# Kernel tuning notes

Hardware: AMD Instinct MI355X
Metric: run time of the kernel (lower is better)

## Reference

```python
import jax, jax.numpy as jnp
import numpy as np

N = 20000      # nodes (atoms)
E = 200000     # directed edges
T = 800000     # triplets
H = 128        # hidden_channels
INT = 64       # int_emb_size
BAS = 8        # basis_emb_size
NS = 7         # num_spherical
NR = 6         # num_radial
OUT = 256      # out_emb_channels
NB = 4         # num_blocks
L = 3          # num_output_layers
CUT = 5.0      # cutoff
silu = jax.nn.silu  # 'swish' activation

# Envelope with exponent=5 -> p=6
_P = 6.0
_A = -(_P + 1.0) * (_P + 2.0) / 2.0   # -28
_B = _P * (_P + 2.0)                  # 48
_C = -_P * (_P + 1.0) / 2.0           # -21

def _envelope(d):
    d5 = d ** 5
    return (1.0 / d + _A * d5 + _B * d5 * d + _C * d5 * d * d) * (d < 1.0).astype(d.dtype)

def setup_inputs() -> dict:
    key = jax.random.key(0)
    ks = iter(jax.random.split(key, 64))
    def p(shape, scale=0.05):
        return jax.random.normal(next(ks), shape, dtype=jnp.float32) * scale
    inp = {}
    inp['z'] = jax.random.randint(next(ks), (N,), 0, 95)
    inp['dist'] = jax.random.uniform(next(ks), (E,), minval=0.1, maxval=CUT, dtype=jnp.float32)
    inp['sbf'] = p((T, NS * NR), 1.0)
    inp['i'] = jax.random.randint(next(ks), (E,), 0, N)
    inp['j'] = jax.random.randint(next(ks), (E,), 0, N)
    inp['idx_kj'] = jax.random.randint(next(ks), (T,), 0, E)
    inp['idx_ji'] = jax.random.randint(next(ks), (T,), 0, E)
    # embedding block params
    s3 = float(np.sqrt(3.0))
    inp['emb_table'] = jax.random.uniform(next(ks), (95, H), minval=-s3, maxval=s3, dtype=jnp.float32)
    inp['W_rbf_emb'] = p((NR, H)); inp['b_rbf_emb'] = jnp.zeros((H,), jnp.float32)
    inp['W_emb'] = p((3 * H, H)); inp['b_emb'] = jnp.zeros((H,), jnp.float32)
    inp['freq'] = jnp.arange(1, NR + 1, dtype=jnp.float32) * jnp.pi
    # interaction blocks (stacked over NB)
    inp['Wi_rbf1'] = p((NB, NR, BAS)); inp['Wi_rbf2'] = p((NB, BAS, H))
    inp['Wi_sbf1'] = p((NB, NS * NR, BAS)); inp['Wi_sbf2'] = p((NB, BAS, INT))
    inp['Wi_kj'] = p((NB, H, H)); inp['bi_kj'] = jnp.zeros((NB, H), jnp.float32)
    inp['Wi_ji'] = p((NB, H, H)); inp['bi_ji'] = jnp.zeros((NB, H), jnp.float32)
    inp['Wi_down'] = p((NB, H, INT)); inp['Wi_up'] = p((NB, INT, H))
    inp['Wi_rb_W1'] = p((NB, H, H)); inp['Wi_rb_b1'] = jnp.zeros((NB, H), jnp.float32)
    inp['Wi_rb_W2'] = p((NB, H, H)); inp['Wi_rb_b2'] = jnp.zeros((NB, H), jnp.float32)
    inp['Wi_lin'] = p((NB, H, H)); inp['bi_lin'] = jnp.zeros((NB, H), jnp.float32)
    inp['Wi_ra_W1'] = p((NB, H, H)); inp['Wi_ra_b1'] = jnp.zeros((NB, H), jnp.float32)
    inp['Wi_ra_W2'] = p((NB, H, H)); inp['Wi_ra_b2'] = jnp.zeros((NB, H), jnp.float32)
    # output blocks (stacked over NB+1)
    inp['Wo_rbf'] = p((NB + 1, NR, H)); inp['Wo_up'] = p((NB + 1, H, OUT))
    inp['Wo_linW'] = p((NB + 1, L, OUT, OUT)); inp['Wo_linb'] = jnp.zeros((NB + 1, L, OUT), jnp.float32)
    return inp

def _forward(z, dist, sbf, i, j, idx_kj, idx_ji,
             emb_table, W_rbf_emb, b_rbf_emb, W_emb, b_emb, freq,
             Wi_rbf1, Wi_rbf2, Wi_sbf1, Wi_sbf2, Wi_kj, bi_kj, Wi_ji, bi_ji,
             Wi_down, Wi_up, Wi_rb_W1, Wi_rb_b1, Wi_rb_W2, Wi_rb_b2,
             Wi_lin, bi_lin, Wi_ra_W1, Wi_ra_b1, Wi_ra_W2, Wi_ra_b2,
             Wo_rbf, Wo_up, Wo_linW, Wo_linb):
    num_nodes = z.shape[0]
    num_edges = dist.shape[0]
    # BesselBasisLayer: rbf [E, NR]
    d = dist / CUT
    rbf = _envelope(d)[:, None] * jnp.sin(freq * d[:, None])
    # EmbeddingBlock -> edge features x [E, H]
    h = emb_table[z]
    rbf_h = silu(rbf @ W_rbf_emb + b_rbf_emb)
    x = silu(jnp.concatenate([h[i], h[j], rbf_h], axis=-1) @ W_emb + b_emb)

    def out_block(b, x_e):
        t = (rbf @ Wo_rbf[b]) * x_e                      # [E, H]
        node = jax.ops.segment_sum(t, i, num_segments=num_nodes)
        node = node @ Wo_up[b]                            # [N, OUT]
        for l in range(L):
            node = silu(node @ Wo_linW[b, l] + Wo_linb[b, l])
        return node

    P = out_block(0, x)
    for b in range(NB):
        # InteractionPPBlock
        x_ji = silu(x @ Wi_ji[b] + bi_ji[b])
        x_kj = silu(x @ Wi_kj[b] + bi_kj[b])
        rbf_b = (rbf @ Wi_rbf1[b]) @ Wi_rbf2[b]           # [E, H]
        x_kj = x_kj * rbf_b
        x_kj = silu(x_kj @ Wi_down[b])                    # [E, INT]
        sbf_b = (sbf @ Wi_sbf1[b]) @ Wi_sbf2[b]           # [T, INT]
        x_kj = x_kj[idx_kj] * sbf_b                       # gather triplets
        x_kj = jax.ops.segment_sum(x_kj, idx_ji, num_segments=num_edges)
        x_kj = silu(x_kj @ Wi_up[b])                      # [E, H]
        hdd = x_ji + x_kj
        # one residual layer before skip (num_before_skip=1)
        hdd = hdd + silu(silu(hdd @ Wi_rb_W1[b] + Wi_rb_b1[b]) @ Wi_rb_W2[b] + Wi_rb_b2[b])
        hdd = silu(hdd @ Wi_lin[b] + bi_lin[b]) + x
        # one residual layer after skip (source uses num_before_skip here too)
        hdd = hdd + silu(silu(hdd @ Wi_ra_W1[b] + Wi_ra_b1[b]) @ Wi_ra_W2[b] + Wi_ra_b2[b])
        x = hdd
        P = P + out_block(b + 1, x)
    return P  # [N, OUT] per-node output embeddings

def reference(z, dist, sbf, i, j, idx_kj, idx_ji,
              emb_table, W_rbf_emb, b_rbf_emb, W_emb, b_emb, freq,
              Wi_rbf1, Wi_rbf2, Wi_sbf1, Wi_sbf2, Wi_kj, bi_kj, Wi_ji, bi_ji,
              Wi_down, Wi_up, Wi_rb_W1, Wi_rb_b1, Wi_rb_W2, Wi_rb_b2,
              Wi_lin, bi_lin, Wi_ra_W1, Wi_ra_b1, Wi_ra_W2, Wi_ra_b2,
              Wo_rbf, Wo_up, Wo_linW, Wo_linb):
    return _forward(z, dist, sbf, i, j, idx_kj, idx_ji,
                    emb_table, W_rbf_emb, b_rbf_emb, W_emb, b_emb, freq,
                    Wi_rbf1, Wi_rbf2, Wi_sbf1, Wi_sbf2, Wi_kj, bi_kj, Wi_ji, bi_ji,
                    Wi_down, Wi_up, Wi_rb_W1, Wi_rb_b1, Wi_rb_W2, Wi_rb_b2,
                    Wi_lin, bi_lin, Wi_ra_W1, Wi_ra_b1, Wi_ra_W2, Wi_ra_b2,
                    Wo_rbf, Wo_up, Wo_linW, Wo_linb)
```

## Files before the change

### kernel.cpp

```cpp
#include <hip/hip_runtime.h>
#include <hip/hip_bf16.h>

#define NND 20000
#define NE  200000
#define NT  800000

#define SW256(row) (((row) & 7) << 4)
#define SW128(row) (((row) & 7) << 4)

typedef short  s16x8 __attribute__((ext_vector_type(8)));
typedef float  f32x4 __attribute__((ext_vector_type(4)));

__device__ __forceinline__ float silu_f(float v) {
    return v * __builtin_amdgcn_rcpf(1.0f + __expf(-v));
}

__device__ __forceinline__ ushort f2bf(float f) {
    uint u = __float_as_uint(f);
    uint r = (u + 0x7FFFu + ((u >> 16) & 1u)) >> 16;
    return (ushort)r;
}
__device__ __forceinline__ float bf2f(ushort u) {
    return __uint_as_float(((uint)u) << 16);
}
__device__ __forceinline__ uint f2bf_pk(float a, float b) {
    __hip_bfloat162 h = __float22bfloat162_rn(make_float2(a, b));
    return *(uint*)&h;
}
__device__ __forceinline__ void store_bf4(void* p, float v0, float v1, float v2, float v3) {
    uint2 o;
    o.x = f2bf_pk(v0, v1);
    o.y = f2bf_pk(v2, v3);
    *(uint2*)p = o;
}

__global__ void rbf_kernel(const float* __restrict__ dist, const float* __restrict__ freq,
                           float* __restrict__ rbf, int E)
{
    int e = blockIdx.x * blockDim.x + threadIdx.x;
    if (e >= E) return;
    float d = dist[e] * 0.2f;
    float d5 = d * d; d5 = d5 * d5 * d;
    float env = 1.0f / d + (-28.0f) * d5 + 48.0f * d5 * d + (-21.0f) * d5 * d * d;
    env = (d < 1.0f) ? env : 0.0f;
    float fr[6];
    #pragma unroll
    for (int r = 0; r < 6; ++r) fr[r] = freq[r];
    #pragma unroll
    for (int r = 0; r < 6; ++r)
        rbf[(size_t)e * 6 + r] = env * sinf(fr[r] * d);
}

__global__ void twt_kernel(const float* __restrict__ W, ushort* __restrict__ Wt,
                           int CIN, int COUT, int total)
{
    int idx = blockIdx.x * 256 + threadIdx.x;
    if (idx >= total) return;
    int per = CIN * COUT;
    int b = idx / per, r = idx % per;
    int k = r / COUT, c = r % COUT;
    Wt[(size_t)b * per + (size_t)c * CIN + k] = f2bf(W[idx]);
}

__global__ void twt7_kernel(const float* __restrict__ s0, const float* __restrict__ s1,
                            const float* __restrict__ s2, const float* __restrict__ s3,
                            const float* __restrict__ s4, const float* __restrict__ s5,
                            const float* __restrict__ s6, ushort* __restrict__ dst)
{
    int idx = blockIdx.x * 256 + threadIdx.x;
    int which = idx >> 16;
    int r = idx & 65535;
    const float* s = (which == 0) ? s0 : (which == 1) ? s1 : (which == 2) ? s2 :
                     (which == 3) ? s3 : (which == 4) ? s4 : (which == 5) ? s5 : s6;
    int b = r >> 14;
    int rr = r & 16383;
    int k = rr >> 7, c = rr & 127;
    dst[(size_t)which * 65536 + b * 16384 + c * 128 + k] = f2bf(s[r]);
}

template<int CIN, int COUT, int MODE, typename IT, typename ET, typename OT>
__global__ __launch_bounds__(256) void mfma_lin_kernel(
    const IT* __restrict__ x, const ushort* __restrict__ Wt,
    const float* __restrict__ bias, const ET* __restrict__ extra,
    OT* __restrict__ y, int M)
{
    constexpr int MT = 64;
    constexpr int NF = COUT / 16;
    constexpr int KS = CIN / 32;
    constexpr int PITCH = CIN * 2;
    __shared__ ushort As_u[MT * CIN];
    __shared__ ushort Ws_u[COUT * CIN];
    char* As = (char*)As_u;
    char* Ws = (char*)Ws_u;
    const int tid = threadIdx.x;
    const int row0 = blockIdx.x * MT;
    const bool full = (row0 + MT <= M);

    constexpr int ACH = MT * CIN / 8;
    for (int c = tid; c < ACH; c += 256) {
        int row = c / (CIN / 8);
        int kc  = c % (CIN / 8);
        int grow = row0 + row;
        s16x8 v;
        if (full || grow < M) {
            if constexpr (sizeof(IT) == 4) {
                const float* src = (const float*)x + (size_t)grow * CIN + kc * 8;
                float4 f0 = *(const float4*)(src);
                float4 f1 = *(const float4*)(src + 4);
                v[0] = (short)f2bf(f0.x); v[1] = (short)f2bf(f0.y);
                v[2] = (short)f2bf(f0.z); v[3] = (short)f2bf(f0.w);
                v[4] = (short)f2bf(f1.x); v[5] = (short)f2bf(f1.y);
                v[6] = (short)f2bf(f1.z); v[7] = (short)f2bf(f1.w);
            } else {
                v = *(const s16x8*)((const ushort*)x + (size_t)grow * CIN + kc * 8);
            }
        } else {
            #pragma unroll
            for (int u = 0; u < 8; ++u) v[u] = 0;
        }
        *(s16x8*)(As + ((row * PITCH + kc * 16) ^ SW256(row))) = v;
    }
    constexpr int WCH = COUT * CIN / 8;
    for (int c = tid; c < WCH; c += 256) {
        int col = c / (CIN / 8);
        int kc  = c % (CIN / 8);
        s16x8 v = *(const s16x8*)(Wt + (size_t)col * CIN + kc * 8);
        *(s16x8*)(Ws + ((col * PITCH + kc * 16) ^ SW256(col))) = v;
    }
    __syncthreads();

    const int w = tid >> 6, lane = tid & 63;
    const int l15 = lane & 15, l4 = lane >> 4;
    const int arow = w * 16 + l15;

    f32x4 acc[NF];
    #pragma unroll
    for (int nf = 0; nf < NF; ++nf) acc[nf] = (f32x4){0.f, 0.f, 0.f, 0.f};

    #pragma unroll
    for (int ks = 0; ks < KS; ++ks) {
        const int kbyte = (ks * 32 + l4 * 8) * 2;
        s16x8 a = *(const s16x8*)(As + ((arow * PITCH + kbyte) ^ SW256(arow)));
        #pragma unroll
        for (int nf = 0; nf < NF; ++nf) {
            int col = nf * 16 + l15;
            s16x8 bf = *(const s16x8*)(Ws + ((col * PITCH + kbyte) ^ SW256(col)));
            acc[nf] = __builtin_amdgcn_mfma_f32_16x16x32_bf16(bf, a, acc[nf], 0, 0, 0);
        }
    }

    const int grow = row0 + w * 16 + l15;
    if (grow < M) {
        #pragma unroll
        for (int nf = 0; nf < NF; ++nf) {
            int c0 = nf * 16 + l4 * 4;
            float4 bv = make_float4(0.f, 0.f, 0.f, 0.f);
            if (bias) bv = *(const float4*)(bias + c0);
            float v0 = acc[nf][0] + bv.x, v1 = acc[nf][1] + bv.y;
            float v2 = acc[nf][2] + bv.z, v3 = acc[nf][3] + bv.w;
            if constexpr (MODE & 1) {
                v0 = silu_f(v0); v1 = silu_f(v1); v2 = silu_f(v2); v3 = silu_f(v3);
            }
            if constexpr ((MODE & 4) != 0) {
                if constexpr (sizeof(ET) == 4) {
                    float4 ex = *(const float4*)((const float*)extra + (size_t)grow * COUT + c0);
                    v0 += ex.x; v1 += ex.y; v2 += ex.z; v3 += ex.w;
                } else {
                    ushort4 ex = *(const ushort4*)((const ushort*)extra + (size_t)grow * COUT + c0);
                    v0 += bf2f(ex.x); v1 += bf2f(ex.y); v2 += bf2f(ex.z); v3 += bf2f(ex.w);
                }
            }
            if constexpr (sizeof(OT) == 4) {
                float* o = (float*)y + (size_t)grow * COUT + c0;
                if constexpr (MODE & 8) {
                    float4 cur = *(const float4*)o;
                    v0 += cur.x; v1 += cur.y; v2 += cur.z; v3 += cur.w;
                }
                *(float4*)o = make_float4(v0, v1, v2, v3);
            } else {
                store_bf4((ushort*)y + (size_t)grow * COUT + c0, v0, v1, v2, v3);
            }
        }
    }
}

__global__ __launch_bounds__(256) void mfma_front_kernel(
    const ushort* __restrict__ x,
    const ushort* __restrict__ Wt1, const ushort* __restrict__ Wt2,
    const ushort* __restrict__ Wtd,
    const float* __restrict__ b1, const float* __restrict__ b2,
    const float* __restrict__ rbf, const float* __restrict__ W1r,
    const float* __restrict__ W2r,
    ushort* __restrict__ y1, ushort* __restrict__ yd, int M)
{
    constexpr int PITCH = 256;
    __shared__ ushort A_u[64 * 128];
    __shared__ ushort W1_u[128 * 128];
    __shared__ ushort W2_u[128 * 128];
    char* A = (char*)A_u;
    char* W1s = (char*)W1_u;
    char* W2s = (char*)W2_u;
    const int tid = threadIdx.x;
    const int row0 = blockIdx.x * 64;

    for (int c = tid; c < 1024; c += 256) {
        int row = c >> 4, kc = c & 15;
        s16x8 v = *(const s16x8*)(x + (size_t)(row0 + row) * 128 + kc * 8);
        *(s16x8*)(A + ((row * PITCH + kc * 16) ^ SW256(row))) = v;
    }
    for (int c = tid; c < 2048; c += 256) {
        int col = c >> 4, kc = c & 15;
        int o = (col * PITCH + kc * 16) ^ SW256(col);
        *(s16x8*)(W1s + o) = *(const s16x8*)(Wt1 + (size_t)col * 128 + kc * 8);
        *(s16x8*)(W2s + o) = *(const s16x8*)(Wt2 + (size_t)col * 128 + kc * 8);
    }
    s16x8 wdreg[4];
    #pragma unroll
    for (int i = 0; i < 4; ++i) {
        int c = tid + i * 256;
        wdreg[i] = *(const s16x8*)(Wtd + (size_t)(c >> 4) * 128 + (c & 15) * 8);
    }
    __syncthreads();

    const int w = tid >> 6, lane = tid & 63;
    const int l15 = lane & 15, l4 = lane >> 4;
    const int arow = w * 16 + l15;

    f32x4 acc1[8], acc2[8];
    #pragma unroll
    for (int nf = 0; nf < 8; ++nf) {
        acc1[nf] = (f32x4){0.f, 0.f, 0.f, 0.f};
        acc2[nf] = (f32x4){0.f, 0.f, 0.f, 0.f};
    }
    #pragma unroll
    for (int ks = 0; ks < 4; ++ks) {
        const int kbyte = (ks * 32 + l4 * 8) * 2;
        s16x8 a = *(const s16x8*)(A + ((arow * PITCH + kbyte) ^ SW256(arow)));
        #pragma unroll
        for (int nf = 0; nf < 8; ++nf) {
            int col = nf * 16 + l15;
            int o = (col * PITCH + kbyte) ^ SW256(col);
            s16x8 bf1 = *(const s16x8*)(W1s + o);
            s16x8 bf2 = *(const s16x8*)(W2s + o);
            acc1[nf] = __builtin_amdgcn_mfma_f32_16x16x32_bf16(bf1, a, acc1[nf], 0, 0, 0);
            acc2[nf] = __builtin_amdgcn_mfma_f32_16x16x32_bf16(bf2, a, acc2[nf], 0, 0, 0);
        }
    }
    __syncthreads();

    const int grow = row0 + arow;
    float rv[6];
    #pragma unroll
    for (int q = 0; q < 6; ++q) rv[q] = rbf[(size_t)grow * 6 + q];
    float t8[8];
    #pragma unroll
    for (int p = 0; p < 8; ++p) {
        float s = 0.f;
        #pragma unroll
        for (int q = 0; q < 6; ++q) s += rv[q] * W1r[q * 8 + p];
        t8[p] = s;
    }
    #pragma unroll
    for (int nf = 0; nf < 8; ++nf) {
        int c0 = nf * 16 + l4 * 4;
        float4 bb1 = *(const float4*)(b1 + c0);
        float4 bb2 = *(const float4*)(b2 + c0);
        store_bf4(y1 + (size_t)grow * 128 + c0,
                  silu_f(acc1[nf][0] + bb1.x), silu_f(acc1[nf][1] + bb1.y),
                  silu_f(acc1[nf][2] + bb1.z), silu_f(acc1[nf][3] + bb1.w));
        float r0 = 0.f, r1 = 0.f, r2 = 0.f, r3 = 0.f;
        #pragma unroll
        for (int p = 0; p < 8; ++p) {
            float4 wq = *(const float4*)(W2r + p * 128 + c0);
            float tp = t8[p];
            r0 += tp * wq.x; r1 += tp * wq.y; r2 += tp * wq.z; r3 += tp * wq.w;
        }
        store_bf4(A + ((arow * PITCH + c0 * 2) ^ SW256(arow)),
                  silu_f(acc2[nf][0] + bb2.x) * r0, silu_f(acc2[nf][1] + bb2.y) * r1,
                  silu_f(acc2[nf][2] + bb2.z) * r2, silu_f(acc2[nf][3] + bb2.w) * r3);
    }
    #pragma unroll
    for (int i = 0; i < 4; ++i) {
        int c = tid + i * 256;
        int col = c >> 4, kc = c & 15;
        *(s16x8*)(W1s + ((col * PITCH + kc * 16) ^ SW256(col))) = wdreg[i];
    }
    __syncthreads();

    f32x4 accd[4];
    #pragma unroll
    for (int nf = 0; nf < 4; ++nf) accd[nf] = (f32x4){0.f, 0.f, 0.f, 0.f};
    #pragma unroll
    for (int ks = 0; ks < 4; ++ks) {
        const int kbyte = (ks * 32 + l4 * 8) * 2;
        s16x8 a = *(const s16x8*)(A + ((arow * PITCH + kbyte) ^ SW256(arow)));
        #pragma unroll
        for (int nf = 0; nf < 4; ++nf) {
            int col = nf * 16 + l15;
            s16x8 bf = *(const s16x8*)(W1s + ((col * PITCH + kbyte) ^ SW256(col)));
            accd[nf] = __builtin_amdgcn_mfma_f32_16x16x32_bf16(bf, a, accd[nf], 0, 0, 0);
        }
    }
    #pragma unroll
    for (int nf = 0; nf < 4; ++nf) {
        int c0 = nf * 16 + l4 * 4;
        store_bf4(yd + (size_t)grow * 64 + c0,
                  silu_f(accd[nf][0]), silu_f(accd[nf][1]),
                  silu_f(accd[nf][2]), silu_f(accd[nf][3]));
    }
}

__global__ __launch_bounds__(256) void mfma_back_kernel(
    const ushort* __restrict__ go, const ushort* __restrict__ xji,
    const ushort* __restrict__ x,
    const ushort* __restrict__ Wup, const ushort* __restrict__ Wrb1,
    const ushort* __restrict__ Wrb2, const ushort* __restrict__ Wlin,
    const ushort* __restrict__ Wra1, const ushort* __restrict__ Wra2,
    const float* __restrict__ b_rb1, const float* __restrict__ b_rb2,
    const float* __restrict__ b_lin, const float* __restrict__ b_ra1,
    const float* __restrict__ b_ra2,
    ushort* __restrict__ xout, int M)
{
    __shared__ ushort A_u[64 * 128];
    __shared__ ushort T_u[64 * 128];
    char* A  = (char*)A_u;
    char* Tb = (char*)T_u;
    const int tid = threadIdx.x;
    const int row0 = blockIdx.x * 64;
    const int w = tid >> 6, lane = tid & 63;
    const int l15 = lane & 15, l4 = lane >> 4;
    const int colbase = w * 32;

    f32x4 acc[8];
    s16x8 wfA[8], wfB[8];
    ushort4 xr[8];

    auto zero_acc = [&]() {
        #pragma unroll
        for (int i = 0; i < 8; ++i) acc[i] = (f32x4){0.f, 0.f, 0.f, 0.f};
    };
    auto load_w8 = [&](s16x8* wf, const ushort* Wg) {
        #pragma unroll
        for (int nfi = 0; nfi < 2; ++nfi)
            #pragma unroll
            for (int ks = 0; ks < 4; ++ks)
                wf[nfi * 4 + ks] = *(const s16x8*)(
                    Wg + (size_t)(colbase + nfi * 16 + l15) * 128 + ks * 32 + l4 * 8);
    };
    auto load_rows = [&](const ushort* src) {
        #pragma unroll
        for (int rt = 0; rt < 4; ++rt) {
            int grow = row0 + rt * 16 + l15;
            #pragma unroll
            for (int nfi = 0; nfi < 2; ++nfi) {
                int c0 = colbase + nfi * 16 + l4 * 4;
                xr[rt * 2 + nfi] = *(const ushort4*)(src + (size_t)grow * 128 + c0);
            }
        }
    };
    auto run_phase = [&](char* Ab, const s16x8* wf) {
        #pragma unroll
        for (int rt = 0; rt < 4; ++rt) {
            int row = rt * 16 + l15;
            #pragma unroll
            for (int ks = 0; ks < 4; ++ks) {
                s16x8 a = *(const s16x8*)(Ab + ((row * 256 + ks * 64 + l4 * 16) ^ SW256(row)));
                acc[rt * 2 + 0] = __builtin_amdgcn_mfma_f32_16x16x32_bf16(wf[0 * 4 + ks], a, acc[rt * 2 + 0], 0, 0, 0);
                acc[rt * 2 + 1] = __builtin_amdgcn_mfma_f32_16x16x32_bf16(wf[1 * 4 + ks], a, acc[rt * 2 + 1], 0, 0, 0);
            }
        }
    };

    s16x8 wfUp[4];
    #pragma unroll
    for (int nfi = 0; nfi < 2; ++nfi)
        #pragma unroll
        for (int ks = 0; ks < 2; ++ks)
            wfUp[nfi * 2 + ks] = *(const s16x8*)(
                Wup + (size_t)(colbase + nfi * 16 + l15) * 64 + ks * 32 + l4 * 8);
    for (int c = tid; c < 512; c += 256) {
        int row = c >> 3, kc = c & 7;
        s16x8 v = *(const s16x8*)(go + (size_t)(row0 + row) * 64 + kc * 8);
        *(s16x8*)(Tb + ((row * 128 + kc * 16) ^ SW128(row))) = v;
    }
    load_w8(wfA, Wrb1);
    load_rows(xji);
    __syncthreads();

    zero_acc();
    #pragma unroll
    for (int rt = 0; rt < 4; ++rt) {
        int row = rt * 16 + l15;
        #pragma unroll
        for (int ks = 0; ks < 2; ++ks) {
            s16x8 a = *(const s16x8*)(Tb + ((row * 128 + ks * 64 + l4 * 16) ^ SW128(row)));
            acc[rt * 2 + 0] = __builtin_amdgcn_mfma_f32_16x16x32_bf16(wfUp[0 * 2 + ks], a, acc[rt * 2 + 0], 0, 0, 0);
            acc[rt * 2 + 1] = __builtin_amdgcn_mfma_f32_16x16x32_bf16(wfUp[1 * 2 + ks], a, acc[rt * 2 + 1], 0, 0, 0);
        }
    }
    #pragma unroll
    for (int rt = 0; rt < 4; ++rt) {
        int row = rt * 16 + l15;
        #pragma unroll
        for (int nfi = 0; nfi < 2; ++nfi) {
            int c0 = colbase + nfi * 16 + l4 * 4;
            f32x4 v = acc[rt * 2 + nfi];
            ushort4 xj = xr[rt * 2 + nfi];
            store_bf4(A + ((row * 256 + c0 * 2) ^ SW256(row)),
                      bf2f(xj.x) + silu_f(v[0]), bf2f(xj.y) + silu_f(v[1]),
                      bf2f(xj.z) + silu_f(v[2]), bf2f(xj.w) + silu_f(v[3]));
        }
    }
    __syncthreads();

    load_w8(wfB, Wrb2);
    zero_acc();
    run_phase(A, wfA);
    #pragma unroll
    for (int rt = 0; rt < 4; ++rt) {
        int row = rt * 16 + l15;
        #pragma unroll
        for (int nfi = 0; nfi < 2; ++nfi) {
            int c0 = colbase + nfi * 16 + l4 * 4;
            f32x4 v = acc[rt * 2 + nfi];
            float4 bb = *(const float4*)(b_rb1 + c0);
            store_bf4(Tb + ((row * 256 + c0 * 2) ^ SW256(row)),
                      silu_f(v[0] + bb.x), silu_f(v[1] + bb.y),
                      silu_f(v[2] + bb.z), silu_f(v[3] + bb.w));
        }
    }
    __syncthreads();

    load_w8(wfA, Wlin);
    load_rows(x);
    zero_acc();
    run_phase(Tb, wfB);
    #pragma unroll
    for (int rt = 0; rt < 4; ++rt) {
        int row = rt * 16 + l15;
        #pragma unroll
        for (int nfi = 0; nfi < 2; ++nfi) {
            int c0 = colbase + nfi * 16 + l4 * 4;
            f32x4 v = acc[rt * 2 + nfi];
            float4 bb = *(const float4*)(b_rb2 + c0);
            int ao = (row * 256 + c0 * 2) ^ SW256(row);
            ushort4 h = *(const ushort4*)(A + ao);
            store_bf4(A + ao,
                      bf2f(h.x) + silu_f(v[0] + bb.x), bf2f(h.y) + silu_f(v[1] + bb.y),
                      bf2f(h.z) + silu_f(v[2] + bb.z), bf2f(h.w) + silu_f(v[3] + bb.w));
        }
    }
    __syncthreads();

    load_w8(wfB, Wra1);
    zero_acc();
    run_phase(A, wfA);
    __syncthreads();
    #pragma unroll
    for (int rt = 0; rt < 4; ++rt) {
        int row = rt * 16 + l15;
        #pragma unroll
        for (int nfi = 0; nfi < 2; ++nfi) {
            int c0 = colbase + nfi * 16 + l4 * 4;
            f32x4 v = acc[rt * 2 + nfi];
            float4 bb = *(const float4*)(b_lin + c0);
            ushort4 xv = xr[rt * 2 + nfi];
            store_bf4(A + ((row * 256 + c0 * 2) ^ SW256(row)),
                      silu_f(v[0] + bb.x) + bf2f(xv.x), silu_f(v[1] + bb.y) + bf2f(xv.y),
                      silu_f(v[2] + bb.z) + bf2f(xv.z), silu_f(v[3] + bb.w) + bf2f(xv.w));
        }
    }
    __syncthreads();

    load_w8(wfA, Wra2);
    zero_acc();
    run_phase(A, wfB);
    #pragma unroll
    for (int rt = 0; rt < 4; ++rt) {
        int row = rt * 16 + l15;
        #pragma unroll
        for (int nfi = 0; nfi < 2; ++nfi) {
            int c0 = colbase + nfi * 16 + l4 * 4;
            f32x4 v = acc[rt * 2 + nfi];
            float4 bb = *(const float4*)(b_ra1 + c0);
            store_bf4(Tb + ((row * 256 + c0 * 2) ^ SW256(row)),
                      silu_f(v[0] + bb.x), silu_f(v[1] + bb.y),
                      silu_f(v[2] + bb.z), silu_f(v[3] + bb.w));
        }
    }
    __syncthreads();

    zero_acc();
    run_phase(Tb, wfA);
    #pragma unroll
    for (int rt = 0; rt < 4; ++rt) {
        int row = rt * 16 + l15;
        int grow = row0 + row;
        #pragma unroll
        for (int nfi = 0; nfi < 2; ++nfi) {
            int c0 = colbase + nfi * 16 + l4 * 4;
            f32x4 v = acc[rt * 2 + nfi];
            float4 bb = *(const float4*)(b_ra2 + c0);
            ushort4 h = *(const ushort4*)(A + ((row * 256 + c0 * 2) ^ SW256(row)));
            store_bf4(xout + (size_t)grow * 128 + c0,
                      bf2f(h.x) + silu_f(v[0] + bb.x), bf2f(h.y) + silu_f(v[1] + bb.y),
                      bf2f(h.z) + silu_f(v[2] + bb.z), bf2f(h.w) + silu_f(v[3] + bb.w));
        }
    }
}

__global__ __launch_bounds__(256) void node_gather_kernel(
    const float* __restrict__ rbf, const float* __restrict__ Wo,
    const ushort* __restrict__ x, const int* __restrict__ noffs,
    const int* __restrict__ nedge, float* __restrict__ node, int N)
{
    const int tid = threadIdx.x;
    const int col = tid & 127;
    const int n = blockIdx.x * 2 + (tid >> 7);
    if (n >= N) return;
    float wo[6];
    #pragma unroll
    for (int q = 0; q < 6; ++q) wo[q] = Wo[q * 128 + col];
    float acc = 0.f;
    const int k0 = noffs[n], k1 = noffs[n + 1];
    for (int k = k0; k < k1; ++k) {
        int e = nedge[k];
        const float* rb = rbf + (size_t)e * 6;
        float t = wo[0] * rb[0] + wo[1] * rb[1] + wo[2] * rb[2]
                + wo[3] * rb[3] + wo[4] * rb[4] + wo[5] * rb[5];
        acc += t * bf2f(x[(size_t)e * 128 + col]);
    }
    node[(size_t)n * 128 + col] = acc;
}

__global__ __launch_bounds__(256) void mfma_out_kernel(
    const float* __restrict__ node,
    const ushort* __restrict__ Wup, const ushort* __restrict__ Wlin,
    const float* __restrict__ BL, float* __restrict__ P, int N)
{
    __shared__ ushort A_u[64 * 256];
    __shared__ ushort T_u[64 * 256];
    __shared__ ushort W_u[128 * 128];
    char* A  = (char*)A_u;
    char* Tb = (char*)T_u;
    char* Ws = (char*)W_u;
    const int tid = threadIdx.x;
    const int row0 = blockIdx.x * 64;
    const int w = tid >> 6, lane = tid & 63;
    const int l15 = lane & 15, l4 = lane >> 4;
    const int arow = w * 16 + l15;
    const int grow = row0 + arow;
    const int c_base = l4 * 4;

    f32x4 acc[16];
    s16x8 wreg[8];

    auto prefetch_w = [&](const ushort* base, int stride) {
        #pragma unroll
        for (int i = 0; i < 8; ++i) {
            int c = tid + i * 256;
            int col = c >> 4, kc = c & 15;
            wreg[i] = *(const s16x8*)(base + (size_t)col * stride + kc * 8);
        }
    };
    auto commit_w = [&]() {
        #pragma unroll
        for (int i = 0; i < 8; ++i) {
            int c = tid + i * 256;
            int col = c >> 4, kc = c & 15;
            *(s16x8*)(Ws + ((col * 256 + kc * 16) ^ SW256(col))) = wreg[i];
        }
    };
    auto run8 = [&](char* Ab, int apitch, int kboff, int accoff) {
        #pragma unroll
        for (int ks = 0; ks < 4; ++ks) {
            const int kbw = ks * 64 + l4 * 16;
            s16x8 a = *(const s16x8*)(Ab + ((arow * apitch + kboff + kbw) ^ SW256(arow)));
            #pragma unroll
            for (int nf = 0; nf < 8; ++nf) {
                int col = nf * 16 + l15;
                s16x8 bf = *(const s16x8*)(Ws + ((col * 256 + kbw) ^ SW256(col)));
                acc[accoff + nf] = __builtin_amdgcn_mfma_f32_16x16x32_bf16(bf, a, acc[accoff + nf], 0, 0, 0);
            }
        }
    };

    #pragma unroll
    for (int i = 0; i < 16; ++i) acc[i] = (f32x4){0.f, 0.f, 0.f, 0.f};

    for (int c = tid; c < 1024; c += 256) {
        int row = c >> 4, kc = c & 15;
        int gr = row0 + row;
        s16x8 v;
        if (gr < N) {
            const float* src = node + (size_t)gr * 128 + kc * 8;
            float4 f0 = *(const float4*)src;
            float4 f1 = *(const float4*)(src + 4);
            v[0] = (short)f2bf(f0.x); v[1] = (short)f2bf(f0.y);
            v[2] = (short)f2bf(f0.z); v[3] = (short)f2bf(f0.w);
            v[4] = (short)f2bf(f1.x); v[5] = (short)f2bf(f1.y);
            v[6] = (short)f2bf(f1.z); v[7] = (short)f2bf(f1.w);
        } else {
            #pragma unroll
            for (int u = 0; u < 8; ++u) v[u] = 0;
        }
        *(s16x8*)(Tb + ((row * 256 + kc * 16) ^ SW256(row))) = v;
    }
    prefetch_w(Wup, 128);
    __syncthreads();
    commit_w();
    prefetch_w(Wup + 128 * 128, 128);
    __syncthreads();
    run8(Tb, 256, 0, 0);
    __syncthreads();
    commit_w();
    prefetch_w(Wlin, 256);
    __syncthreads();
    run8(Tb, 256, 0, 8);
    #pragma unroll
    for (int nf = 0; nf < 16; ++nf) {
        int c0 = nf * 16 + c_base;
        store_bf4(A + ((arow * 512 + c0 * 2) ^ SW256(arow)),
                  acc[nf][0], acc[nf][1], acc[nf][2], acc[nf][3]);
    }
    __syncthreads();

    char* S = A; char* D = Tb;
    for (int l = 0; l < 3; ++l) {
        #pragma unroll
        for (int i = 0; i < 16; ++i) acc[i] = (f32x4){0.f, 0.f, 0.f, 0.f};
        const ushort* WL = Wlin + (size_t)l * 65536;
        for (int q = 0; q < 4; ++q) {
            int ch = q & 1, kh = q >> 1;
            commit_w();
            if (q < 3) {
                int nq = q + 1;
                prefetch_w(WL + (size_t)(nq & 1) * 128 * 256 + (nq >> 1) * 128, 256);
            } else if (l < 2) {
                prefetch_w(Wlin + (size_t)(l + 1) * 65536, 256);
            }
            __syncthreads();
            run8(S, 512, kh * 256, ch * 8);
            __syncthreads();
        }
        const float* bl = BL + l * 256;
        if (l < 2) {
            #pragma unroll
            for (int nf = 0; nf < 16; ++nf) {
                int c0 = nf * 16 + c_base;
                float4 bb = *(const float4*)(bl + c0);
                store_bf4(D + ((arow * 512 + c0 * 2) ^ SW256(arow)),
                          silu_f(acc[nf][0] + bb.x), silu_f(acc[nf][1] + bb.y),
                          silu_f(acc[nf][2] + bb.z), silu_f(acc[nf][3] + bb.w));
            }
            __syncthreads();
            char* tmp = S; S = D; D = tmp;
        } else if (grow < N) {
            #pragma unroll
            for (int nf = 0; nf < 16; ++nf) {
                int c0 = nf * 16 + c_base;
                float4 bb = *(const float4*)(bl + c0);
                float* o = P + (size_t)grow * 256 + c0;
                float4 cur = *(const float4*)o;
                *(float4*)o = make_float4(cur.x + silu_f(acc[nf][0] + bb.x),
                                          cur.y + silu_f(acc[nf][1] + bb.y),
                                          cur.z + silu_f(acc[nf][2] + bb.z),
                                          cur.w + silu_f(acc[nf][3] + bb.w));
            }
        }
    }
}

template<int CIN, int COUT, int MODE, typename OT>
__global__ __launch_bounds__(256) void lin_kernel(
    const float* __restrict__ x, const float* __restrict__ W,
    const float* __restrict__ bias, const float* __restrict__ extra,
    OT* __restrict__ y, int M)
{
    constexpr int MT = 64;
    constexpr int CG = COUT / 4;
    constexpr int RG = 256 / CG;
    constexpr int MR = MT / RG;
    __shared__ float xs[MT * CIN];

    const int row0 = blockIdx.x * MT;
    const int tid  = threadIdx.x;
    const int rem  = M - row0;

    if (rem >= MT) {
        const float4* src = (const float4*)(x + (size_t)row0 * CIN);
        constexpr int TOT4 = (MT * CIN) / 4;
        for (int idx = tid; idx < TOT4; idx += 256)
            ((float4*)xs)[idx] = src[idx];
    } else {
        for (int idx = tid; idx < MT * CIN; idx += 256) {
            int r = idx / CIN;
            xs[idx] = (r < rem) ? x[(size_t)(row0 + r) * CIN + (idx % CIN)] : 0.0f;
        }
    }
    __syncthreads();

    const int cg = tid % CG, rg = tid / CG;
    const int c0 = cg * 4;
    float acc[MR][4];
    #pragma unroll
    for (int m = 0; m < MR; ++m) { acc[m][0]=0; acc[m][1]=0; acc[m][2]=0; acc[m][3]=0; }

    for (int k = 0; k < CIN; ++k) {
        float4 w = *(const float4*)(W + (size_t)k * COUT + c0);
        #pragma unroll
        for (int m = 0; m < MR; ++m) {
            float xv = xs[(rg * MR + m) * CIN + k];
            acc[m][0] += xv * w.x; acc[m][1] += xv * w.y;
            acc[m][2] += xv * w.z; acc[m][3] += xv * w.w;
        }
    }

    float4 bv = make_float4(0.f, 0.f, 0.f, 0.f);
    if (bias) bv = *(const float4*)(bias + c0);

    #pragma unroll
    for (int m = 0; m < MR; ++m) {
        int row = row0 + rg * MR + m;
        if (row >= M) continue;
        float v[4] = { acc[m][0] + bv.x, acc[m][1] + bv.y, acc[m][2] + bv.z, acc[m][3] + bv.w };
        if constexpr (MODE & 1) {
            #pragma unroll
            for (int u = 0; u < 4; ++u) v[u] = silu_f(v[u]);
        }
        if constexpr (sizeof(OT) == 4) {
            *(float4*)((float*)y + (size_t)row * COUT + c0) = make_float4(v[0], v[1], v[2], v[3]);
        } else {
            store_bf4((ushort*)y + (size_t)row * COUT + c0, v[0], v[1], v[2], v[3]);
        }
    }
}

__global__ __launch_bounds__(256) void fuse_embed_kernel(
    const int* __restrict__ z, const int* __restrict__ ii, const int* __restrict__ jj,
    const float* __restrict__ pt1, const float* __restrict__ pt2,
    const ushort* __restrict__ t3, const float* __restrict__ bias,
    ushort* __restrict__ x, int E)
{
    int idx = blockIdx.x * 256 + threadIdx.x;
    int e = idx >> 5;
    if (e >= E) return;
    int c4 = (idx & 31) * 4;
    int zi = z[ii[e]], zj = z[jj[e]];
    float4 a = *(const float4*)(pt1 + zi * 128 + c4);
    float4 b = *(const float4*)(pt2 + zj * 128 + c4);
    ushort4 t = *(const ushort4*)(t3 + (size_t)e * 128 + c4);
    float4 bb = *(const float4*)(bias + c4);
    store_bf4(x + (size_t)e * 128 + c4,
              silu_f(a.x + b.x + bf2f(t.x) + bb.x), silu_f(a.y + b.y + bf2f(t.y) + bb.y),
              silu_f(a.z + b.z + bf2f(t.z) + bb.z), silu_f(a.w + b.w + bf2f(t.w) + bb.w));
}

__global__ __launch_bounds__(256) void s1all_kernel(
    const float* __restrict__ sbf, const float* __restrict__ W1,
    const int* __restrict__ pos, ushort* __restrict__ s1all, int T)
{
    constexpr int TT = 32;
    constexpr int FL = TT * 42;
    __shared__ float s_flat[FL];
    __shared__ float s_w1[4 * 42 * 8];
    __shared__ ushort s_out[TT][4][8];
    const int t0 = blockIdx.x * TT;
    const int tid = threadIdx.x;

    for (int k = tid; k < 4 * 42 * 8; k += 256) s_w1[k] = W1[k];
    if (t0 + TT <= T) {
        const float4* src = (const float4*)(sbf + (size_t)t0 * 42);
        for (int k = tid; k < FL / 4; k += 256)
            ((float4*)s_flat)[k] = src[k];
    } else {
        const size_t base = (size_t)t0 * 42;
        const size_t tot = (size_t)T * 42;
        for (int k = tid; k < FL; k += 256)
            s_flat[k] = (base + k < tot) ? sbf[base + k] : 0.0f;
    }
    __syncthreads();
    {
        int t = tid >> 3, p = tid & 7;
        const float* row = s_flat + t * 42;
        float a0 = 0.f, a1 = 0.f, a2 = 0.f, a3 = 0.f;
        #pragma unroll
        for (int q = 0; q < 42; ++q) {
            float xv = row[q];
            a0 += xv * s_w1[0 * 336 + q * 8 + p];
            a1 += xv * s_w1[1 * 336 + q * 8 + p];
            a2 += xv * s_w1[2 * 336 + q * 8 + p];
            a3 += xv * s_w1[3 * 336 + q * 8 + p];
        }
        s_out[t][0][p] = f2bf(a0);
        s_out[t][1][p] = f2bf(a1);
        s_out[t][2][p] = f2bf(a2);
        s_out[t][3][p] = f2bf(a3);
    }
    __syncthreads();
    if (tid < 128) {
        int t = tid >> 2, b = tid & 3;
        int gt = t0 + t;
        if (gt < T)
            *(s16x8*)(s1all + ((size_t)pos[gt] * 4 + b) * 8) = *(const s16x8*)s_out[t][b];
    }
}

__global__ void count_kernel(const int* __restrict__ seg, int* __restrict__ deg, int T)
{
    int t = blockIdx.x * blockDim.x + threadIdx.x;
    if (t < T) atomicAdd(&deg[seg[t]], 1);
}

__global__ __launch_bounds__(256) void scan1_kernel(const int* __restrict__ deg,
                                                    int* __restrict__ offs,
                                                    int* __restrict__ bsum, int E)
{
    __shared__ int s[256];
    int tid = threadIdx.x;
    int g = blockIdx.x * 256 + tid;
    int v = (g < E) ? deg[g] : 0;
    s[tid] = v;
    __syncthreads();
    for (int d = 1; d < 256; d <<= 1) {
        int t = (tid >= d) ? s[tid - d] : 0;
        __syncthreads();
        s[tid] += t;
        __syncthreads();
    }
    if (g < E) offs[g] = s[tid] - v;
    if (tid == 255) bsum[blockIdx.x] = s[255];
}

__global__ __launch_bounds__(1024) void scan2_kernel(int* __restrict__ bsum, int NB)
{
    __shared__ int s[1024];
    int tid = threadIdx.x;
    int v = (tid < NB) ? bsum[tid] : 0;
    s[tid] = v;
    __syncthreads();
    for (int d = 1; d < 1024; d <<= 1) {
        int t = (tid >= d) ? s[tid - d] : 0;
        __syncthreads();
        s[tid] += t;
        __syncthreads();
    }
    if (tid < NB) bsum[tid] = s[tid] - v;
}

__global__ __launch_bounds__(256) void scan3_kernel(int* __restrict__ offs,
                                                    const int* __restrict__ bsum,
                                                    int E, int T)
{
    int g = blockIdx.x * 256 + threadIdx.x;
    if (g < E) offs[g] += bsum[blockIdx.x];
    if (g == 0) offs[E] = T;
}

__global__ void fill_kernel(const int* __restrict__ idx_ji, const int* __restrict__ idx_kj,
                            const int* __restrict__ offs, int* __restrict__ cursor,
                            int* __restrict__ kj_csr, int* __restrict__ pos, int T)
{
    int t = blockIdx.x * blockDim.x + threadIdx.x;
    if (t >= T) return;
    int ji = idx_ji[t];
    int slot = atomicAdd(&cursor[ji], 1);
    int k = offs[ji] + slot;
    kj_csr[k] = idx_kj[t];
    pos[t] = k;
}

__global__ void fillN_kernel(const int* __restrict__ ii, const int* __restrict__ offs,
                             int* __restrict__ cursor, int* __restrict__ elist, int E)
{
    int e = blockIdx.x * blockDim.x + threadIdx.x;
    if (e >= E) return;
    int n = ii[e];
    int slot = atomicAdd(&cursor[n], 1);
    elist[offs[n] + slot] = e;
}

__global__ __launch_bounds__(256) void gather2_kernel(
    const ushort* __restrict__ s1, const float* __restrict__ W2,
    const ushort* __restrict__ xd, const int* __restrict__ kj_csr,
    const int* __restrict__ offs, ushort* __restrict__ out, int E, int boff)
{
    const int lane = threadIdx.x & 63;
    const int e = blockIdx.x * 4 + (threadIdx.x >> 6);
    if (e >= E) return;
    float w2[8];
    #pragma unroll
    for (int p = 0; p < 8; ++p) w2[p] = W2[p * 64 + lane];
    float accA = 0.0f, accB = 0.0f;
    const int k0 = offs[e], k1 = offs[e + 1];
    int k = k0;
    for (; k + 1 < k1; k += 2) {
        s16x8 sv0 = *(const s16x8*)(s1 + (size_t)k * 32 + boff);
        s16x8 sv1 = *(const s16x8*)(s1 + (size_t)(k + 1) * 32 + boff);
        int kj0 = kj_csr[k];
        int kj1 = kj_csr[k + 1];
        float x0 = bf2f(xd[(size_t)kj0 * 64 + lane]);
        float x1 = bf2f(xd[(size_t)kj1 * 64 + lane]);
        float sb0 = bf2f((ushort)sv0[0]) * w2[0] + bf2f((ushort)sv0[1]) * w2[1]
                  + bf2f((ushort)sv0[2]) * w2[2] + bf2f((ushort)sv0[3]) * w2[3]
                  + bf2f((ushort)sv0[4]) * w2[4] + bf2f((ushort)sv0[5]) * w2[5]
                  + bf2f((ushort)sv0[6]) * w2[6] + bf2f((ushort)sv0[7]) * w2[7];
        float sb1 = bf2f((ushort)sv1[0]) * w2[0] + bf2f((ushort)sv1[1]) * w2[1]
                  + bf2f((ushort)sv1[2]) * w2[2] + bf2f((ushort)sv1[3]) * w2[3]
                  + bf2f((ushort)sv1[4]) * w2[4] + bf2f((ushort)sv1[5]) * w2[5]
                  + bf2f((ushort)sv1[6]) * w2[6] + bf2f((ushort)sv1[7]) * w2[7];
        accA += sb0 * x0;
        accB += sb1 * x1;
    }
    if (k < k1) {
        s16x8 sv = *(const s16x8*)(s1 + (size_t)k * 32 + boff);
        int kj = kj_csr[k];
        float sb = bf2f((ushort)sv[0]) * w2[0] + bf2f((ushort)sv[1]) * w2[1]
                 + bf2f((ushort)sv[2]) * w2[2] + bf2f((ushort)sv[3]) * w2[3]
                 + bf2f((ushort)sv[4]) * w2[4] + bf2f((ushort)sv[5]) * w2[5]
                 + bf2f((ushort)sv[6]) * w2[6] + bf2f((ushort)sv[7]) * w2[7];
        accA += sb * bf2f(xd[(size_t)kj * 64 + lane]);
    }
    out[(size_t)e * 64 + lane] = f2bf(accA + accB);
}

extern "C" void kernel_launch(void* const* d_in, const int* in_sizes, int n_in,
                              void* d_out, int out_size, void* d_ws, size_t ws_size,
                              hipStream_t stream)
{
    const int*   z         = (const int*)  d_in[0];
    const float* dist      = (const float*)d_in[1];
    const float* sbf       = (const float*)d_in[2];
    const int*   ii        = (const int*)  d_in[3];
    const int*   jj        = (const int*)  d_in[4];
    const int*   idx_kj    = (const int*)  d_in[5];
    const int*   idx_ji    = (const int*)  d_in[6];
    const float* emb_table = (const float*)d_in[7];
    const float* W_rbf_emb = (const float*)d_in[8];
    const float* b_rbf_emb = (const float*)d_in[9];
    const float* W_emb     = (const float*)d_in[10];
    const float* b_emb     = (const float*)d_in[11];
    const float* freq      = (const float*)d_in[12];
    const float* Wi_rbf1   = (const float*)d_in[13];
    const float* Wi_rbf2   = (const float*)d_in[14];
    const float* Wi_sbf1   = (const float*)d_in[15];
    const float* Wi_sbf2   = (const float*)d_in[16];
    const float* Wi_kj     = (const float*)d_in[17];
    const float* bi_kj     = (const float*)d_in[18];
    const float* Wi_ji     = (const float*)d_in[19];
    const float* bi_ji     = (const float*)d_in[20];
    const float* Wi_down   = (const float*)d_in[21];
    const float* Wi_up     = (const float*)d_in[22];
    const float* Wi_rb_W1  = (const float*)d_in[23];
    const float* Wi_rb_b1  = (const float*)d_in[24];
    const float* Wi_rb_W2  = (const float*)d_in[25];
    const float* Wi_rb_b2  = (const float*)d_in[26];
    const float* Wi_lin    = (const float*)d_in[27];
    const float* bi_lin    = (const float*)d_in[28];
    const float* Wi_ra_W1  = (const float*)d_in[29];
    const float* Wi_ra_b1  = (const float*)d_in[30];
    const float* Wi_ra_W2  = (const float*)d_in[31];
    const float* Wi_ra_b2  = (const float*)d_in[32];
    const float* Wo_rbf    = (const float*)d_in[33];
    const float* Wo_up     = (const float*)d_in[34];
    const float* Wo_linW   = (const float*)d_in[35];
    const float* Wo_linb   = (const float*)d_in[36];

    const int N = NND, E = NE, T = NT;
    float* ws = (float*)d_ws;
    size_t off = 0;
    float* rbf  = ws + off; off += (size_t)E * 6;
    float* buf0 = ws + off; off += (size_t)E * 128;
    float* buf1 = ws + off; off += (size_t)E * 128;
    float* buf2 = ws + off; off += (size_t)E * 128;
    float* buf3 = ws + off; off += (size_t)E * 64;
    float* buf4 = ws + off; off += (size_t)E * 64;
    int* ideg  = (int*)(ws + off); off += E;
    int* ioffs = (int*)(ws + off); off += E + 1;
    int* icur  = (int*)(ws + off); off += E;
    int* ikj   = (int*)(ws + off); off += T;
    int* ipos  = (int*)(ws + off); off += T;
    int* ibsum = (int*)(ws + off); off += 1024;
    int* ndeg  = (int*)(ws + off); off += N;
    int* noffs = (int*)(ws + off); off += N + 1;
    int* ncur  = (int*)(ws + off); off += N;
    int* nedge = (int*)(ws + off); off += E;
    int* nbsum = (int*)(ws + off); off += 1024;
    float* pt1 = ws + off; off += 95 * 128;
    float* pt2 = ws + off; off += 95 * 128;
    ushort* wt_ji   = (ushort*)(ws + off);
    ushort* wt_kj   = wt_ji   + 4 * 16384;
    ushort* wt_rb1  = wt_kj   + 4 * 16384;
    ushort* wt_rb2  = wt_rb1  + 4 * 16384;
    ushort* wt_lin  = wt_rb2  + 4 * 16384;
    ushort* wt_ra1  = wt_lin  + 4 * 16384;
    ushort* wt_ra2  = wt_ra1  + 4 * 16384;
    ushort* wt_down = wt_ra2  + 4 * 16384;
    ushort* wt_up   = wt_down + 4 * 8192;
    ushort* wt_emb3 = wt_up   + 4 * 8192;
    ushort* wt_oup  = wt_emb3 + 16384;
    ushort* wt_olin = wt_oup  + 5 * 32768;
    off += (7 * 4 * 16384 + 2 * 4 * 8192 + 16384 + 5 * 32768 + 15 * 65536 + 1) / 2;

    ushort* xb     = (ushort*)buf0;
    ushort* xjib   = (ushort*)buf1;
    ushort* rbfhb  = (ushort*)buf2;
    ushort* t3b    = (ushort*)buf1;
    ushort* s1all  = (ushort*)buf2;
    ushort* xdb    = (ushort*)buf3;
    ushort* gob    = (ushort*)buf4;
    float*  node   = buf3;
    float* P = (float*)d_out;

    const int gridE  = (E + 63) / 64;
    const int gridN  = (N + 63) / 64;
    const int NB_SCAN  = (E + 255) / 256;
    const int NB_SCANN = (N + 255) / 256;

    hipMemsetAsync(d_out, 0, (size_t)N * 256 * 4, stream);

    twt7_kernel<<<7 * 65536 / 256, 256, 0, stream>>>(
        Wi_ji, Wi_kj, Wi_rb_W1, Wi_rb_W2, Wi_lin, Wi_ra_W1, Wi_ra_W2, wt_ji);
    twt_kernel<<<128, 256, 0, stream>>>(Wi_down,  wt_down, 128,  64, 4 * 8192);
    twt_kernel<<<128, 256, 0, stream>>>(Wi_up,    wt_up,    64, 128, 4 * 8192);
    twt_kernel<<<64,  256, 0, stream>>>(W_emb + 256 * 128, wt_emb3, 128, 128, 16384);
    twt_kernel<<<640, 256, 0, stream>>>(Wo_up,   wt_oup,  128, 256, 5 * 32768);
    twt_kernel<<<3840, 256, 0, stream>>>(Wo_linW, wt_olin, 256, 256, 15 * 65536);

    hipMemsetAsync(ideg, 0, (size_t)E * 4, stream);
    count_kernel<<<(T + 255) / 256, 256, 0, stream>>>(idx_ji, ideg, T);
    scan1_kernel<<<NB_SCAN, 256, 0, stream>>>(ideg, ioffs, ibsum, E);
    scan2_kernel<<<1, 1024, 0, stream>>>(ibsum, NB_SCAN);
    scan3_kernel<<<NB_SCAN, 256, 0, stream>>>(ioffs, ibsum, E, T);
    hipMemsetAsync(icur, 0, (size_t)E * 4, stream);
    fill_kernel<<<(T + 255) / 256, 256, 0, stream>>>(idx_ji, idx_kj, ioffs, icur, ikj, ipos, T);

    hipMemsetAsync(ndeg, 0, (size_t)N * 4, stream);
    count_kernel<<<(E + 255) / 256, 256, 0, stream>>>(ii, ndeg, E);
    scan1_kernel<<<NB_SCANN, 256, 0, stream>>>(ndeg, noffs, nbsum, N);
    scan2_kernel<<<1, 1024, 0, stream>>>(nbsum, NB_SCANN);
    scan3_kernel<<<NB_SCANN, 256, 0, stream>>>(noffs, nbsum, N, E);
    hipMemsetAsync(ncur, 0, (size_t)N * 4, stream);
    fillN_kernel<<<(E + 255) / 256, 256, 0, stream>>>(ii, noffs, ncur, nedge, E);

    rbf_kernel<<<(E + 255) / 256, 256, 0, stream>>>(dist, freq, rbf, E);
    lin_kernel<6, 128, 1, ushort><<<gridE, 256, 0, stream>>>(rbf, W_rbf_emb, b_rbf_emb, nullptr, rbfhb, E);
    lin_kernel<128, 128, 0, float><<<2, 256, 0, stream>>>(emb_table, W_emb, nullptr, nullptr, pt1, 95);
    lin_kernel<128, 128, 0, float><<<2, 256, 0, stream>>>(emb_table, W_emb + 128 * 128, nullptr, nullptr, pt2, 95);
    mfma_lin_kernel<128, 128, 0, ushort, float, ushort><<<gridE, 256, 0, stream>>>(
        rbfhb, wt_emb3, nullptr, nullptr, t3b, E);
    fuse_embed_kernel<<<(E * 32 + 255) / 256, 256, 0, stream>>>(z, ii, jj, pt1, pt2, t3b, b_emb, xb, E);
    s1all_kernel<<<(T + 31) / 32, 256, 0, stream>>>(sbf, Wi_sbf1, ipos, s1all, T);

    auto out_block = [&](int b) {
        node_gather_kernel<<<(N + 1) / 2, 256, 0, stream>>>(
            rbf, Wo_rbf + (size_t)b * 6 * 128, xb, noffs, nedge, node, N);
        mfma_out_kernel<<<gridN, 256, 0, stream>>>(
            node, wt_oup + (size_t)b * 32768, wt_olin + (size_t)b * 3 * 65536,
            Wo_linb + (size_t)b * 3 * 256, P, N);
    };

    out_block(0);

    for (int b = 0; b < 4; ++b) {
        mfma_front_kernel<<<gridE, 256, 0, stream>>>(
            xb, wt_ji + (size_t)b * 16384, wt_kj + (size_t)b * 16384,
            wt_down + (size_t)b * 8192,
            bi_ji + b * 128, bi_kj + b * 128,
            rbf, Wi_rbf1 + (size_t)b * 48, Wi_rbf2 + (size_t)b * 1024,
            xjib, xdb, E);
        gather2_kernel<<<(E + 3) / 4, 256, 0, stream>>>(
            s1all, Wi_sbf2 + (size_t)b * 512, xdb, ikj, ioffs, gob, E, b * 8);
        mfma_back_kernel<<<gridE, 256, 0, stream>>>(
            gob, xjib, xb,
            wt_up + (size_t)b * 8192, wt_rb1 + (size_t)b * 16384,
            wt_rb2 + (size_t)b * 16384, wt_lin + (size_t)b * 16384,
            wt_ra1 + (size_t)b * 16384, wt_ra2 + (size_t)b * 16384,
            Wi_rb_b1 + b * 128, Wi_rb_b2 + b * 128, bi_lin + b * 128,
            Wi_ra_b1 + b * 128, Wi_ra_b2 + b * 128,
            xb, E);

        out_block(b + 1);
    }
}
```

Baseline: 1.927 ms.

## Keep front-kernel weight fragments in registers instead of staging weights in LDS

The front MFMA kernel no longer copies the two 128x128 weight matrices and the down-projection weights into shared memory. Each wave now owns a 32-column slice of outputs across all 64 rows, so it loads its weight fragments straight from global memory into registers and streams only the activation tile from LDS. This cuts LDS use from about 80KB to 16KB per block, which should allow more resident blocks and removes the large weight staging. In exchange every block re-reads weights from global or L2 memory and uses more registers.

Measured after the change: 2.114 ms. 9.7% more time.

```diff
diff --git a/kernel.cpp b/kernel.cpp
--- a/kernel.cpp
+++ b/kernel.cpp
@@ -193,120 +193,125 @@
     const float* __restrict__ W2r,
     ushort* __restrict__ y1, ushort* __restrict__ yd, int M)
 {
-    constexpr int PITCH = 256;
     __shared__ ushort A_u[64 * 128];
-    __shared__ ushort W1_u[128 * 128];
-    __shared__ ushort W2_u[128 * 128];
     char* A = (char*)A_u;
-    char* W1s = (char*)W1_u;
-    char* W2s = (char*)W2_u;
     const int tid = threadIdx.x;
     const int row0 = blockIdx.x * 64;
+    const int w = tid >> 6, lane = tid & 63;
+    const int l15 = lane & 15, l4 = lane >> 4;
+    const int colbase = w * 32;
+
+    f32x4 acc1[8], acc2[8];
+    s16x8 wf[8];
+
+    auto load_w8 = [&](const ushort* Wg) {
+        #pragma unroll
+        for (int nfi = 0; nfi < 2; ++nfi)
+            #pragma unroll
+            for (int ks = 0; ks < 4; ++ks)
+                wf[nfi * 4 + ks] = *(const s16x8*)(
+                    Wg + (size_t)(colbase + nfi * 16 + l15) * 128 + ks * 32 + l4 * 8);
+    };
 
     for (int c = tid; c < 1024; c += 256) {
         int row = c >> 4, kc = c & 15;
         s16x8 v = *(const s16x8*)(x + (size_t)(row0 + row) * 128 + kc * 8);
-        *(s16x8*)(A + ((row * PITCH + kc * 16) ^ SW256(row))) = v;
-    }
-    for (int c = tid; c < 2048; c += 256) {
-        int col = c >> 4, kc = c & 15;
-        int o = (col * PITCH + kc * 16) ^ SW256(col);
-        *(s16x8*)(W1s + o) = *(const s16x8*)(Wt1 + (size_t)col * 128 + kc * 8);
-        *(s16x8*)(W2s + o) = *(const s16x8*)(Wt2 + (size_t)col * 128 + kc * 8);
-    }
-    s16x8 wdreg[4];
-    #pragma unroll
-    for (int i = 0; i < 4; ++i) {
-        int c = tid + i * 256;
-        wdreg[i] = *(const s16x8*)(Wtd + (size_t)(c >> 4) * 128 + (c & 15) * 8);
-    }
-    __syncthreads();
-
-    const int w = tid >> 6, lane = tid & 63;
-    const int l15 = lane & 15, l4 = lane >> 4;
-    const int arow = w * 16 + l15;
-
-    f32x4 acc1[8], acc2[8];
-    #pragma unroll
-    for (int nf = 0; nf < 8; ++nf) {
-        acc1[nf] = (f32x4){0.f, 0.f, 0.f, 0.f};
-        acc2[nf] = (f32x4){0.f, 0.f, 0.f, 0.f};
-    }
-    #pragma unroll
-    for (int ks = 0; ks < 4; ++ks) {
-        const int kbyte = (ks * 32 + l4 * 8) * 2;
-        s16x8 a = *(const s16x8*)(A + ((arow * PITCH + kbyte) ^ SW256(arow)));
-        #pragma unroll
-        for (int nf = 0; nf < 8; ++nf) {
-            int col = nf * 16 + l15;
-            int o = (col * PITCH + kbyte) ^ SW256(col);
-            s16x8 bf1 = *(const s16x8*)(W1s + o);
-            s16x8 bf2 = *(const s16x8*)(W2s + o);
-            acc1[nf] = __builtin_amdgcn_mfma_f32_16x16x32_bf16(bf1, a, acc1[nf], 0, 0, 0);
-            acc2[nf] = __builtin_amdgcn_mfma_f32_16x16x32_bf16(bf2, a, acc2[nf], 0, 0, 0);
-        }
-    }
-    __syncthreads();
-
-    const int grow = row0 + arow;
-    float rv[6];
-    #pragma unroll
-    for (int q = 0; q < 6; ++q) rv[q] = rbf[(size_t)grow * 6 + q];
-    float t8[8];
-    #pragma unroll
-    for (int p = 0; p < 8; ++p) {
-        float s = 0.f;
-        #pragma unroll
-        for (int q = 0; q < 6; ++q) s += rv[q] * W1r[q * 8 + p];
-        t8[p] = s;
-    }
-    #pragma unroll
-    for (int nf = 0; nf < 8; ++nf) {
-        int c0 = nf * 16 + l4 * 4;
-        float4 bb1 = *(const float4*)(b1 + c0);
-        float4 bb2 = *(const float4*)(b2 + c0);
-        store_bf4(y1 + (size_t)grow * 128 + c0,
-                  silu_f(acc1[nf][0] + bb1.x), silu_f(acc1[nf][1] + bb1.y),
-                  silu_f(acc1[nf][2] + bb1.z), silu_f(acc1[nf][3] + bb1.w));
-        float r0 = 0.f, r1 = 0.f, r2 = 0.f, r3 = 0.f;
+        *(s16x8*)(A + ((row * 256 + kc * 16) ^ SW256(row))) = v;
+    }
+    load_w8(Wt1);
+    __syncthreads();
+
+    #pragma unroll
+    for (int i = 0; i < 8; ++i) {
+        acc1[i] = (f32x4){0.f, 0.f, 0.f, 0.f};
+        acc2[i] = (f32x4){0.f, 0.f, 0.f, 0.f};
+    }
+
+    #pragma unroll
+    for (int rt = 0; rt < 4; ++rt) {
+        int row = rt * 16 + l15;
+        #pragma unroll
+        for (int ks = 0; ks < 4; ++ks) {
+            s16x8 a = *(const s16x8*)(A + ((row * 256 + ks * 64 + l4 * 16) ^ SW256(row)));
+            acc1[rt * 2 + 0] = __builtin_amdgcn_mfma_f32_16x16x32_bf16(wf[0 * 4 + ks], a, acc1[rt * 2 + 0], 0, 0, 0);
+            acc1[rt * 2 + 1] = __builtin_amdgcn_mfma_f32_16x16x32_bf16(wf[1 * 4 + ks], a, acc1[rt * 2 + 1], 0, 0, 0);
+        }
+    }
+    load_w8(Wt2);
+    #pragma unroll
+    for (int rt = 0; rt < 4; ++rt) {
+        int row = rt * 16 + l15;
+        #pragma unroll
+        for (int ks = 0; ks < 4; ++ks) {
+            s16x8 a = *(const s16x8*)(A + ((row * 256 + ks * 64 + l4 * 16) ^ SW256(row)));
+            acc2[rt * 2 + 0] = __builtin_amdgcn_mfma_f32_16x16x32_bf16(wf[0 * 4 + ks], a, acc2[rt * 2 + 0], 0, 0, 0);
+            acc2[rt * 2 + 1] = __builtin_amdgcn_mfma_f32_16x16x32_bf16(wf[1 * 4 + ks], a, acc2[rt * 2 + 1], 0, 0, 0);
+        }
+    }
+    __syncthreads();
+
+    #pragma unroll
+    for (int rt = 0; rt < 4; ++rt) {
+        int row = rt * 16 + l15;
+        int grow = row0 + row;
+        float rv[6];
+        #pragma unroll
+        for (int q = 0; q < 6; ++q) rv[q] = rbf[(size_t)grow * 6 + q];
+        float t8[8];
         #pragma unroll
         for (int p = 0; p < 8; ++p) {
-            float4 wq = *(const float4*)(W2r + p * 128 + c0);
-            float tp = t8[p];
-            r0 += tp * wq.x; r1 += tp * wq.y; r2 += tp * wq.z; r3 += tp * wq.w;
-        }
-        store_bf4(A + ((arow * PITCH + c0 * 2) ^ SW256(arow)),
-                  silu_f(acc2[nf][0] + bb2.x) * r0, silu_f(acc2[nf][1] + bb2.y) * r1,
-                  silu_f(acc2[nf][2] + bb2.z) * r2, silu_f(acc2[nf][3] + bb2.w) * r3);
-    }
-    #pragma unroll
-    for (int i = 0; i < 4; ++i) {
-        int c = tid + i * 256;
-        int col = c >> 4, kc = c & 15;
-        *(s16x8*)(W1s + ((col * PITCH + kc * 16) ^ SW256(col))) = wdreg[i];
-    }
+            float s = 0.f;
+            #pragma unroll
+            for (int q = 0; q < 6; ++q) s += rv[q] * W1r[q * 8 + p];
+            t8[p] = s;
+        }
+        #pragma unroll
+        for (int nfi = 0; nfi < 2; ++nfi) {
+            int c0 = colbase + nfi * 16 + l4 * 4;
+            f32x4 v1 = acc1[rt * 2 + nfi];
+            f32x4 v2 = acc2[rt * 2 + nfi];
+            float4 bb1 = *(const float4*)(b1 + c0);
+            float4 bb2 = *(const float4*)(b2 + c0);
+            store_bf4(y1 + (size_t)grow * 128 + c0,
+                      silu_f(v1[0] + bb1.x), silu_f(v1[1] + bb1.y),
+                      silu_f(v1[2] + bb1.z), silu_f(v1[3] + bb1.w));
+            float r0 = 0.f, r1 = 0.f, r2 = 0.f, r3 = 0.f;
+            #pragma unroll
+            for (int p = 0; p < 8; ++p) {
+                float4 wq = *(const float4*)(W2r + p * 128 + c0);
+                float tp = t8[p];
+                r0 += tp * wq.x; r1 += tp * wq.y; r2 += tp * wq.z; r3 += tp * wq.w;
+            }
+            store_bf4(A + ((row * 256 + c0 * 2) ^ SW256(row)),
+                      silu_f(v2[0] + bb2.x) * r0, silu_f(v2[1] + bb2.y) * r1,
+                      silu_f(v2[2] + bb2.z) * r2, silu_f(v2[3] + bb2.w) * r3);
+        }
+    }
+    s16x8 wfd[4];
+    #pragma unroll
+    for (int ks = 0; ks < 4; ++ks)
+        wfd[ks] = *(const s16x8*)(Wtd + (size_t)(w * 16 + l15) * 128 + ks * 32 + l4 * 8);
     __syncthreads();
 
     f32x4 accd[4];
     #pragma unroll
-    for (int nf = 0; nf < 4; ++nf) accd[nf] = (f32x4){0.f, 0.f, 0.f, 0.f};
-    #pragma unroll
-    for (int ks = 0; ks < 4; ++ks) {
-        const int kbyte = (ks * 32 + l4 * 8) * 2;
-        s16x8 a = *(const s16x8*)(A + ((arow * PITCH + kbyte) ^ SW256(arow)));
-        #pragma unroll
-        for (int nf = 0; nf < 4; ++nf) {
-            int col = nf * 16 + l15;
-            s16x8 bf = *(const s16x8*)(W1s + ((col * PITCH + kbyte) ^ SW256(col)));
-            accd[nf] = __builtin_amdgcn_mfma_f32_16x16x32_bf16(bf, a, accd[nf], 0, 0, 0);
-        }
-    }
-    #pragma unroll
-    for (int nf = 0; nf < 4; ++nf) {
-        int c0 = nf * 16 + l4 * 4;
+    for (int i = 0; i < 4; ++i) accd[i] = (f32x4){0.f, 0.f, 0.f, 0.f};
+    #pragma unroll
+    for (int rt = 0; rt < 4; ++rt) {
+        int row = rt * 16 + l15;
+        #pragma unroll
+        for (int ks = 0; ks < 4; ++ks) {
+            s16x8 a = *(const s16x8*)(A + ((row * 256 + ks * 64 + l4 * 16) ^ SW256(row)));
+            accd[rt] = __builtin_amdgcn_mfma_f32_16x16x32_bf16(wfd[ks], a, accd[rt], 0, 0, 0);
+        }
+    }
+    #pragma unroll
+    for (int rt = 0; rt < 4; ++rt) {
+        int grow = row0 + rt * 16 + l15;
+        int c0 = w * 16 + l4 * 4;
         store_bf4(yd + (size_t)grow * 64 + c0,
-                  silu_f(accd[nf][0]), silu_f(accd[nf][1]),
-                  silu_f(accd[nf][2]), silu_f(accd[nf][3]));
+                  silu_f(accd[rt][0]), silu_f(accd[rt][1]),
+                  silu_f(accd[rt][2]), silu_f(accd[rt][3]));
     }
 }
 
```
